# Optimization experiments

Hardware: AMD Instinct MI355X
Metric: run time of the kernel (lower is better)

Reference implementation:

```python
import jax, jax.numpy as jnp
import numpy as np

PATCH = 14          # config.patch_size
MAX_SEQ = 2048      # config.max_vit_seq_len
A2 = 4              # adaptor_patch_size ** 2
GRID = 32           # max_image_size // patch_size -> sqrt(num_positions - 1)
EPS = 1e-5          # layer_norm_eps

IMG_SIZES = [(448, 448), (448, 672), (336, 336), (224, 448), (560, 560), (336, 448)]


def bilinear_resize_chw(img, oh, ow):
    # torch F.interpolate(mode='bilinear', align_corners=False): half-pixel centers, edge clamp
    C, H, W = img.shape
    def coords(o, i):
        c = (jnp.arange(o, dtype=jnp.float32) + 0.5) * (i / o) - 0.5
        c = jnp.clip(c, 0.0, i - 1.0)
        lo = jnp.floor(c).astype(jnp.int32)
        hi = jnp.minimum(lo + 1, i - 1)
        return lo, hi, c - lo
    y0, y1, wy = coords(oh, H)
    x0, x1, wx = coords(ow, W)
    top = img[:, y0][:, :, x0] * (1 - wx) + img[:, y0][:, :, x1] * wx
    bot = img[:, y1][:, :, x0] * (1 - wx) + img[:, y1][:, :, x1] * wx
    wy = wy[None, :, None]
    return top * (1 - wy) + bot * wy


def patch_embed(img, conv_w, conv_b):
    # Conv2d(k=stride=PATCH) == non-overlapping patch extract + matmul
    C, H, W = img.shape
    h, w = H // PATCH, W // PATCH
    x = img[:, :h * PATCH, :w * PATCH].reshape(C, h, PATCH, w, PATCH)
    x = x.transpose(1, 3, 0, 2, 4).reshape(h * w, C * PATCH * PATCH)  # [hw, c*kh*kw]
    out = x @ conv_w.reshape(conv_w.shape[0], -1).T + conv_b          # [hw, E]
    return out, (h, w)


def pos_embed_interp(pos_table, h, w):
    pe = pos_table[1:]  # drop cls position, [GRID*GRID, E]
    if (h, w) == (GRID, GRID):
        return pe
    E = pe.shape[-1]
    pe2d = pe.reshape(GRID, GRID, E).transpose(2, 0, 1)  # [E, GRID, GRID]
    pe2d = bilinear_resize_chw(pe2d, h, w)
    return pe2d.transpose(1, 2, 0).reshape(h * w, E)


def layernorm(x, g, b):
    m = x.mean(-1, keepdims=True)
    v = ((x - m) ** 2).mean(-1, keepdims=True)
    return (x - m) / jnp.sqrt(v + EPS) * g + b


def pack_positions(hw_list):
    # static replay of group_images_by_max_seq_len + a2 rescale in forward
    pos, batch_idx, seq_len = [], 0, 0
    for (h, w) in hw_list:
        L = h * w
        if seq_len + L > MAX_SEQ:
            batch_idx += 1
            seq_len = 0
        s = (seq_len // A2) * A2
        pos.append((batch_idx, s, s + (L // A2) * A2))
        seq_len += L
    return pos, batch_idx + 1


def setup_inputs() -> dict:
    key = jax.random.key(0)
    ks = jax.random.split(key, 9)
    E = 1280
    inp = {}
    for i, (H, W) in enumerate(IMG_SIZES):
        inp[f'img{i}'] = jax.random.normal(ks[i], (3, H, W), dtype=jnp.float32)
    inp['conv_w'] = jax.random.normal(ks[6], (E, 3, PATCH, PATCH), dtype=jnp.float32) * 0.02
    inp['conv_b'] = jnp.zeros((E,), dtype=jnp.float32)
    inp['pos_table'] = jax.random.normal(ks[7], (GRID * GRID + 1, E), dtype=jnp.float32) * 0.02
    inp['ln_w'] = jnp.ones((E,), dtype=jnp.float32)
    inp['ln_b'] = jnp.zeros((E,), dtype=jnp.float32)
    return inp


def reference(img0, img1, img2, img3, img4, img5, conv_w, conv_b, pos_table, ln_w, ln_b):
    images = [img0, img1, img2, img3, img4, img5]
    E = conv_w.shape[0]
    hw = [(im.shape[1] // PATCH, im.shape[2] // PATCH) for im in images]
    positions, B = pack_positions(hw)
    emb = jnp.zeros((B, MAX_SEQ, E), dtype=jnp.float32)
    mask = np.zeros((B, 1, MAX_SEQ, MAX_SEQ), dtype=bool)
    for im, (bi, s, e) in zip(images, positions):
        x, (h, w) = patch_embed(im, conv_w, conv_b)
        x = x + pos_embed_interp(pos_table, h, w)
        x = layernorm(x, ln_w, ln_b)
        emb = emb.at[bi, s:e].set(x)
        mask[bi, 0, s:e, s:e] = True
    return emb, jnp.asarray(mask)
```

## Files before the change

### kernel.cpp

```cpp
#include <hip/hip_runtime.h>
#include <hip/hip_bf16.h>
#include <stdint.h>

#define E_DIM 1280
#define KDIM 588
#define KPAD 608
#define M_TOTAL 6016
#define EMB_FLOATS (5*2048*1280)
#define MASK_FLOATS (5*2048*2048)

#define EXT_BLOCKS  3572
#define CW_BLOCKS   760
#define ZERO_BLOCKS 1320
#define MASK_BLOCKS 5120
#define TOTAL_BLOCKS (EXT_BLOCKS + CW_BLOCKS + ZERO_BLOCKS + MASK_BLOCKS)

typedef __attribute__((ext_vector_type(8))) short bf16x8;
typedef __attribute__((ext_vector_type(4))) float f32x4;

struct us4 { unsigned short x, y, z, w; };

__device__ __forceinline__ unsigned short f2bf(float f) {
    unsigned int u = __float_as_uint(f);
    u += 0x7fff + ((u >> 16) & 1);
    return (unsigned short)(u >> 16);
}

template<int PW, int IMGW, int PLANE>
__device__ __forceinline__ void do_extract4(const float* __restrict__ img,
                                            us4* __restrict__ A4,
                                            int base_u4, int local_u4)
{
    int r_local = local_u4 / 152;
    int k4 = (local_u4 - r_local * 152) * 4;
    us4 v = {0, 0, 0, 0};
    if (k4 < KDIM) {
        int py = r_local / PW;  int px = r_local - py * PW;
        int c   = k4 / 196;
        int rem0 = k4 - c * 196;
        const float* p = img + (size_t)c * PLANE;
        unsigned short o[4];
        #pragma unroll
        for (int j = 0; j < 4; ++j) {
            int rem = rem0 + j;
            int iy = rem / 14, ix = rem - iy * 14;
            o[j] = f2bf(p[(size_t)(py*14 + iy) * IMGW + (px*14 + ix)]);
        }
        v.x = o[0]; v.y = o[1]; v.z = o[2]; v.w = o[3];
    }
    A4[base_u4 + local_u4] = v;
}

__global__ __launch_bounds__(256) void fused_prep(
    const float* __restrict__ i0, const float* __restrict__ i1,
    const float* __restrict__ i2, const float* __restrict__ i3,
    const float* __restrict__ i4, const float* __restrict__ i5,
    const float* __restrict__ conv_w,
    us4* __restrict__ A4, us4* __restrict__ W4,
    float4* __restrict__ out4)
{
    const int bid = blockIdx.x;
    const int t = threadIdx.x;

    if (bid < EXT_BLOCKS) {
        if (bid < 608) {
            do_extract4<32,448,200704>(i0, A4, 0,      bid * 256 + t);
        } else if (bid < 1520) {
            do_extract4<48,672,301056>(i1, A4, 155648, (bid - 608) * 256 + t);
        } else if (bid < 1862) {
            do_extract4<24,336,112896>(i2, A4, 389120, (bid - 1520) * 256 + t);
        } else if (bid < 2166) {
            do_extract4<32,448,100352>(i3, A4, 476672, (bid - 1862) * 256 + t);
        } else if (bid < 3116) {
            do_extract4<40,560,313600>(i4, A4, 554496, (bid - 2166) * 256 + t);
        } else {
            do_extract4<32,448,150528>(i5, A4, 797696, (bid - 3116) * 256 + t);
        }
    } else if (bid < EXT_BLOCKS + CW_BLOCKS) {
        int idx4 = (bid - EXT_BLOCKS) * 256 + t;
        int e  = idx4 / 152;
        int k4 = (idx4 - e * 152) * 4;
        us4 v = {0, 0, 0, 0};
        if (k4 < KDIM) {
            const float* p = conv_w + (size_t)e * KDIM + k4;
            v.x = f2bf(p[0]); v.y = f2bf(p[1]); v.z = f2bf(p[2]); v.w = f2bf(p[3]);
        }
        W4[idx4] = v;
    } else if (bid < EXT_BLOCKS + CW_BLOCKS + ZERO_BLOCKS) {
        int base = (bid - EXT_BLOCKS - CW_BLOCKS) * 1024 + t;
        #pragma unroll
        for (int j = 0; j < 4; ++j) {
            int idx = base + j * 256;
            int zrow = idx / 320;
            int c4   = idx - zrow * 320;
            int b, rowInB;
            if      (zrow < 1024) { b = 0; rowInB = 1024 + zrow; }
            else if (zrow < 1536) { b = 1; rowInB = 1536 + (zrow - 1024); }
            else if (zrow < 2496) { b = 2; rowInB = 1088 + (zrow - 1536); }
            else if (zrow < 2944) { b = 3; rowInB = 1600 + (zrow - 2496); }
            else                  { b = 4; rowInB =  768 + (zrow - 2944); }
            size_t o4 = ((size_t)(b * 2048 + rowInB) * E_DIM) / 4 + c4;
            out4[o4] = make_float4(0.f, 0.f, 0.f, 0.f);
        }
    } else {
        int base = (bid - EXT_BLOCKS - CW_BLOCKS - ZERO_BLOCKS) * 1024 + t;
        #pragma unroll
        for (int j = 0; j < 4; ++j) {
            int m4 = base + j * 256;
            int b  = m4 >> 20;
            int rr = (m4 >> 9) & 2047;
            int c0 = (m4 & 511) * 4;
            int h0 = (b == 0) ? 1024 : (b == 1) ? 1536 : (b == 2) ? 576 : (b == 3) ? 1600 : 768;
            bool on = (rr < h0 && c0 < h0);
            if (b == 2) on = on || (rr >= 576 && rr < 1088 && c0 >= 576 && c0 < 1088);
            float f = on ? 1.f : 0.f;
            out4[(size_t)(EMB_FLOATS / 4) + m4] = make_float4(f, f, f, f);
        }
    }
}

__global__ __launch_bounds__(256) void gemm_bf16(
    const unsigned short* __restrict__ A,
    const unsigned short* __restrict__ Bm,
    float* __restrict__ C)
{
    __shared__ __align__(16) unsigned short As[128*32];
    __shared__ __align__(16) unsigned short Bs[128*32];
    const int t  = threadIdx.x;
    const int m0 = blockIdx.x * 128;
    const int n0 = blockIdx.y * 128;
    const int lane = t & 63;
    const int wv = t >> 6;
    const int wr = wv >> 1, wc = wv & 1;
    const int l16 = lane & 15, q = lane >> 4;

    f32x4 acc[4][4] = {};

    for (int kk = 0; kk < KPAD; kk += 32) {
        #pragma unroll
        for (int i = 0; i < 2; ++i) {
            int off = i * 4096 + t * 16;
            int row = off >> 6;
            int kb  = (off & 63) >> 1;
            const unsigned short* ga = A  + (size_t)(m0 + row) * KPAD + kk + kb;
            __builtin_amdgcn_global_load_lds(
                (const __attribute__((address_space(1))) void*)ga,
                (__attribute__((address_space(3))) void*)((char*)As + off), 16, 0, 0);
            const unsigned short* gb = Bm + (size_t)(n0 + row) * KPAD + kk + kb;
            __builtin_amdgcn_global_load_lds(
                (const __attribute__((address_space(1))) void*)gb,
                (__attribute__((address_space(3))) void*)((char*)Bs + off), 16, 0, 0);
        }
        __syncthreads();

        bf16x8 af[4], bfr[4];
        #pragma unroll
        for (int mi = 0; mi < 4; ++mi)
            af[mi] = *(const bf16x8*)&As[(wr*64 + mi*16 + l16) * 32 + q * 8];
        #pragma unroll
        for (int ni = 0; ni < 4; ++ni)
            bfr[ni] = *(const bf16x8*)&Bs[(wc*64 + ni*16 + l16) * 32 + q * 8];
        #pragma unroll
        for (int mi = 0; mi < 4; ++mi)
            #pragma unroll
            for (int ni = 0; ni < 4; ++ni)
                acc[mi][ni] = __builtin_amdgcn_mfma_f32_16x16x32_bf16(
                    af[mi], bfr[ni], acc[mi][ni], 0, 0, 0);
        __syncthreads();
    }

    #pragma unroll
    for (int mi = 0; mi < 4; ++mi) {
        #pragma unroll
        for (int ni = 0; ni < 4; ++ni) {
            int col = n0 + wc*64 + ni*16 + l16;
            #pragma unroll
            for (int reg = 0; reg < 4; ++reg) {
                int rowr = m0 + wr*64 + mi*16 + q*4 + reg;
                C[(size_t)rowr * E_DIM + col] = acc[mi][ni][reg];
            }
        }
    }
}

__global__ __launch_bounds__(256) void epilogue(
    const float* __restrict__ C, const float* __restrict__ pos_table,
    const float* __restrict__ conv_b,
    const float* __restrict__ ln_w, const float* __restrict__ ln_b,
    float* __restrict__ out)
{
    const int t = threadIdx.x;
    const int wave = t >> 6, lane = t & 63;
    const int r = blockIdx.x * 4 + wave;

    int img     = (r < 1024) ? 0 : (r < 2560) ? 1 : (r < 3136) ? 2 : (r < 3648) ? 3 : (r < 5248) ? 4 : 5;
    int rowOff  = (img == 0) ? 0 : (img == 1) ? 1024 : (img == 2) ? 2560 : (img == 3) ? 3136 : (img == 4) ? 3648 : 5248;
    int h       = (img == 0) ? 32 : (img == 1) ? 32 : (img == 2) ? 24 : (img == 3) ? 16 : (img == 4) ? 40 : 24;
    int w       = (img == 0) ? 32 : (img == 1) ? 48 : (img == 2) ? 24 : (img == 3) ? 32 : (img == 4) ? 40 : 32;
    int outBase = (img == 0) ? 0 : (img == 1) ? 2048 : (img == 2) ? 4096 : (img == 3) ? 4672 : (img == 4) ? 6144 : 8192;

    int ri = r - rowOff;
    int y = ri / w, x = ri - y * w;

    float cy = fminf(fmaxf((y + 0.5f) * (32.0f / h) - 0.5f, 0.0f), 31.0f);
    float cx = fminf(fmaxf((x + 0.5f) * (32.0f / w) - 0.5f, 0.0f), 31.0f);
    int y0 = (int)floorf(cy); int y1 = min(y0 + 1, 31); float wy = cy - (float)y0;
    int x0 = (int)floorf(cx); int x1 = min(x0 + 1, 31); float wx = cx - (float)x0;

    const float4* P00 = (const float4*)(pos_table + (size_t)(1 + y0*32 + x0) * E_DIM);
    const float4* P01 = (const float4*)(pos_table + (size_t)(1 + y0*32 + x1) * E_DIM);
    const float4* P10 = (const float4*)(pos_table + (size_t)(1 + y1*32 + x0) * E_DIM);
    const float4* P11 = (const float4*)(pos_table + (size_t)(1 + y1*32 + x1) * E_DIM);
    const float4* C4  = (const float4*)(C + (size_t)r * E_DIM);
    const float4* B4  = (const float4*)conv_b;

    float w00 = (1.f - wy) * (1.f - wx), w01 = (1.f - wy) * wx;
    float w10 = wy * (1.f - wx),         w11 = wy * wx;

    float4 vals[5];
    float s = 0.f, s2 = 0.f;
    #pragma unroll
    for (int j = 0; j < 5; ++j) {
        int e4 = lane + j * 64;
        float4 a = P00[e4], b2 = P01[e4], c2 = P10[e4], d2 = P11[e4];
        float4 cv = C4[e4], bv = B4[e4];
        float4 v;
        v.x = cv.x + bv.x + w00*a.x + w01*b2.x + w10*c2.x + w11*d2.x;
        v.y = cv.y + bv.y + w00*a.y + w01*b2.y + w10*c2.y + w11*d2.y;
        v.z = cv.z + bv.z + w00*a.z + w01*b2.z + w10*c2.z + w11*d2.z;
        v.w = cv.w + bv.w + w00*a.w + w01*b2.w + w10*c2.w + w11*d2.w;
        vals[j] = v;
        s  += v.x + v.y + v.z + v.w;
        s2 += v.x*v.x + v.y*v.y + v.z*v.z + v.w*v.w;
    }
    #pragma unroll
    for (int m = 32; m > 0; m >>= 1) {
        s  += __shfl_xor(s,  m, 64);
        s2 += __shfl_xor(s2, m, 64);
    }
    float mean = s / 1280.f;
    float var  = s2 / 1280.f - mean * mean;
    float inv  = 1.f / sqrtf(var + 1e-5f);

    float4* O4 = (float4*)(out + (size_t)(outBase + ri) * E_DIM);
    #pragma unroll
    for (int j = 0; j < 5; ++j) {
        int e4 = lane + j * 64;
        float4 g = ((const float4*)ln_w)[e4], be = ((const float4*)ln_b)[e4];
        float4 v = vals[j], o4;
        o4.x = (v.x - mean) * inv * g.x + be.x;
        o4.y = (v.y - mean) * inv * g.y + be.y;
        o4.z = (v.z - mean) * inv * g.z + be.z;
        o4.w = (v.w - mean) * inv * g.w + be.w;
        O4[e4] = o4;
    }
}

extern "C" void kernel_launch(void* const* d_in, const int* in_sizes, int n_in,
                              void* d_out, int out_size, void* d_ws, size_t ws_size,
                              hipStream_t stream) {
    const float* img0 = (const float*)d_in[0];
    const float* img1 = (const float*)d_in[1];
    const float* img2 = (const float*)d_in[2];
    const float* img3 = (const float*)d_in[3];
    const float* img4 = (const float*)d_in[4];
    const float* img5 = (const float*)d_in[5];
    const float* conv_w    = (const float*)d_in[6];
    const float* conv_b    = (const float*)d_in[7];
    const float* pos_table = (const float*)d_in[8];
    const float* ln_w      = (const float*)d_in[9];
    const float* ln_b      = (const float*)d_in[10];
    float* out = (float*)d_out;

    unsigned short* Abf = (unsigned short*)d_ws;
    unsigned short* Wbf = Abf + (size_t)M_TOTAL * KPAD;
    float* Cbuf = (float*)(Wbf + (size_t)E_DIM * KPAD);

    fused_prep<<<TOTAL_BLOCKS, 256, 0, stream>>>(
        img0, img1, img2, img3, img4, img5, conv_w,
        (us4*)Abf, (us4*)Wbf, (float4*)out);

    dim3 g(M_TOTAL / 128, E_DIM / 128);
    gemm_bf16<<<g, 256, 0, stream>>>(Abf, Wbf, Cbuf);

    epilogue<<<1504, 256, 0, stream>>>(Cbuf, pos_table, conv_b, ln_w, ln_b, out);
}
```

Baseline: 206.4 us.

## Fuse GEMM with pos-embed and LayerNorm epilogue, co-schedule mask/zero fill

Replaces the separate LDS-tiled GEMM and epilogue kernels with one kernel. Each block computes a full 32x1280 row strip using direct global-to-register double-buffered fragment loads, then applies bias, bilinear position embedding and LayerNorm in registers with a cross-wave reduction through shared memory. The zero and mask fills move from the prep kernel into this kernel's grid as extra blocks. This drops the fp32 C buffer round trip and one launch. The cost is that the GEMM runs on only 188 blocks and reads unstaged, uncoalesced fragments from global memory.

```diff
diff --git a/kernel.cpp b/kernel.cpp
--- a/kernel.cpp
+++ b/kernel.cpp
@@ -11,9 +11,12 @@
 
 #define EXT_BLOCKS  3572
 #define CW_BLOCKS   760
-#define ZERO_BLOCKS 1320
-#define MASK_BLOCKS 5120
-#define TOTAL_BLOCKS (EXT_BLOCKS + CW_BLOCKS + ZERO_BLOCKS + MASK_BLOCKS)
+#define PREP_BLOCKS (EXT_BLOCKS + CW_BLOCKS)
+
+#define GEMM_BLOCKS 188
+#define ZERO_BLOCKS2 660
+#define MASK_BLOCKS2 2560
+#define FUSED_BLOCKS (GEMM_BLOCKS + ZERO_BLOCKS2 + MASK_BLOCKS2)
 
 typedef __attribute__((ext_vector_type(8))) short bf16x8;
 typedef __attribute__((ext_vector_type(4))) float f32x4;
@@ -51,17 +54,15 @@
     A4[base_u4 + local_u4] = v;
 }
 
-__global__ __launch_bounds__(256) void fused_prep(
+__global__ __launch_bounds__(256) void prep(
     const float* __restrict__ i0, const float* __restrict__ i1,
     const float* __restrict__ i2, const float* __restrict__ i3,
     const float* __restrict__ i4, const float* __restrict__ i5,
     const float* __restrict__ conv_w,
-    us4* __restrict__ A4, us4* __restrict__ W4,
-    float4* __restrict__ out4)
+    us4* __restrict__ A4, us4* __restrict__ W4)
 {
     const int bid = blockIdx.x;
     const int t = threadIdx.x;
-
     if (bid < EXT_BLOCKS) {
         if (bid < 608) {
             do_extract4<32,448,200704>(i0, A4, 0,      bid * 256 + t);
@@ -76,7 +77,7 @@
         } else {
             do_extract4<32,448,150528>(i5, A4, 797696, (bid - 3116) * 256 + t);
         }
-    } else if (bid < EXT_BLOCKS + CW_BLOCKS) {
+    } else {
         int idx4 = (bid - EXT_BLOCKS) * 256 + t;
         int e  = idx4 / 152;
         int k4 = (idx4 - e * 152) * 4;
@@ -86,11 +87,141 @@
             v.x = f2bf(p[0]); v.y = f2bf(p[1]); v.z = f2bf(p[2]); v.w = f2bf(p[3]);
         }
         W4[idx4] = v;
-    } else if (bid < EXT_BLOCKS + CW_BLOCKS + ZERO_BLOCKS) {
-        int base = (bid - EXT_BLOCKS - CW_BLOCKS) * 1024 + t;
+    }
+}
+
+__global__ __launch_bounds__(512) void fused_gemm(
+    const unsigned short* __restrict__ A,
+    const unsigned short* __restrict__ Wb,
+    const float* __restrict__ pos_table, const float* __restrict__ conv_b,
+    const float* __restrict__ ln_w, const float* __restrict__ ln_b,
+    float* __restrict__ out, float4* __restrict__ out4)
+{
+    const int bid = blockIdx.x;
+    const int t = threadIdx.x;
+
+    if (bid < GEMM_BLOCKS) {
+        const int m0   = bid * 32;
+        const int wave = t >> 6;
+        const int lane = t & 63;
+        const int l16  = lane & 15, q = lane >> 4;
+        const int ncol0 = wave * 160;
+
+        f32x4 acc[2][10] = {};
+        const unsigned short* ap = A  + (size_t)(m0 + l16) * KPAD + q * 8;
+        const unsigned short* bp = Wb + (size_t)(ncol0 + l16) * KPAD + q * 8;
+
+        bf16x8 ab[2][2], bb[2][10];
+        #pragma unroll
+        for (int mi = 0; mi < 2; ++mi) ab[0][mi] = *(const bf16x8*)(ap + mi * 16 * KPAD);
+        #pragma unroll
+        for (int ni = 0; ni < 10; ++ni) bb[0][ni] = *(const bf16x8*)(bp + ni * 16 * KPAD);
+
+        #pragma unroll
+        for (int kki = 0; kki < 19; ++kki) {
+            const int cur = kki & 1, nxt = cur ^ 1;
+            if (kki < 18) {
+                const unsigned short* apn = ap + (kki + 1) * 32;
+                const unsigned short* bpn = bp + (kki + 1) * 32;
+                #pragma unroll
+                for (int mi = 0; mi < 2; ++mi) ab[nxt][mi] = *(const bf16x8*)(apn + mi * 16 * KPAD);
+                #pragma unroll
+                for (int ni = 0; ni < 10; ++ni) bb[nxt][ni] = *(const bf16x8*)(bpn + ni * 16 * KPAD);
+            }
+            #pragma unroll
+            for (int mi = 0; mi < 2; ++mi)
+                #pragma unroll
+                for (int ni = 0; ni < 10; ++ni)
+                    acc[mi][ni] = __builtin_amdgcn_mfma_f32_16x16x32_bf16(
+                        ab[cur][mi], bb[cur][ni], acc[mi][ni], 0, 0, 0);
+        }
+
+        int img     = (m0 < 1024) ? 0 : (m0 < 2560) ? 1 : (m0 < 3136) ? 2 : (m0 < 3648) ? 3 : (m0 < 5248) ? 4 : 5;
+        int rowOff  = (img == 0) ? 0 : (img == 1) ? 1024 : (img == 2) ? 2560 : (img == 3) ? 3136 : (img == 4) ? 3648 : 5248;
+        int h       = (img == 0) ? 32 : (img == 1) ? 32 : (img == 2) ? 24 : (img == 3) ? 16 : (img == 4) ? 40 : 24;
+        int w       = (img == 0) ? 32 : (img == 1) ? 48 : (img == 2) ? 24 : (img == 3) ? 32 : (img == 4) ? 40 : 32;
+        int outBase = (img == 0) ? 0 : (img == 1) ? 2048 : (img == 2) ? 4096 : (img == 3) ? 4672 : (img == 4) ? 6144 : 8192;
+        unsigned int magic = (unsigned int)((1u << 22) / (unsigned)w) + 1u;
+        float sh = 32.0f / (float)h, sw = 32.0f / (float)w;
+
+        float cbv[10], gv[10], bev[10];
+        #pragma unroll
+        for (int ni = 0; ni < 10; ++ni) {
+            int col = ncol0 + ni * 16 + l16;
+            cbv[ni] = conv_b[col];
+            gv[ni]  = ln_w[col];
+            bev[ni] = ln_b[col];
+        }
+
+        __shared__ float part_s[8][32], part_s2[8][32], ln_m[32], ln_i[32];
+
+        #pragma unroll
+        for (int mi = 0; mi < 2; ++mi) {
+            #pragma unroll
+            for (int reg = 0; reg < 4; ++reg) {
+                int row_t = mi * 16 + q * 4 + reg;
+                int ri = m0 + row_t - rowOff;
+                unsigned int y = ((unsigned int)ri * magic) >> 22;
+                int x = ri - (int)y * w;
+                float cy = fminf(fmaxf(((float)y + 0.5f) * sh - 0.5f, 0.0f), 31.0f);
+                float cx = fminf(fmaxf(((float)x + 0.5f) * sw - 0.5f, 0.0f), 31.0f);
+                int y0 = (int)cy; int y1 = min(y0 + 1, 31); float wy = cy - (float)y0;
+                int x0 = (int)cx; int x1 = min(x0 + 1, 31); float wx = cx - (float)x0;
+                float w00 = (1.f - wy) * (1.f - wx), w01 = (1.f - wy) * wx;
+                float w10 = wy * (1.f - wx),         w11 = wy * wx;
+                const float* P00 = pos_table + (size_t)(1 + y0*32 + x0) * E_DIM;
+                const float* P01 = pos_table + (size_t)(1 + y0*32 + x1) * E_DIM;
+                const float* P10 = pos_table + (size_t)(1 + y1*32 + x0) * E_DIM;
+                const float* P11 = pos_table + (size_t)(1 + y1*32 + x1) * E_DIM;
+                float s = 0.f, s2 = 0.f;
+                #pragma unroll
+                for (int ni = 0; ni < 10; ++ni) {
+                    int col = ncol0 + ni * 16 + l16;
+                    float p = w00*P00[col] + w01*P01[col] + w10*P10[col] + w11*P11[col];
+                    float v = acc[mi][ni][reg] + cbv[ni] + p;
+                    acc[mi][ni][reg] = v;
+                    s += v; s2 += v * v;
+                }
+                #pragma unroll
+                for (int msk = 1; msk < 16; msk <<= 1) {
+                    s  += __shfl_xor(s,  msk, 64);
+                    s2 += __shfl_xor(s2, msk, 64);
+                }
+                if (l16 == 0) { part_s[wave][row_t] = s; part_s2[wave][row_t] = s2; }
+            }
+        }
+        __syncthreads();
+        if (t < 32) {
+            float S = 0.f, S2 = 0.f;
+            #pragma unroll
+            for (int w2 = 0; w2 < 8; ++w2) { S += part_s[w2][t]; S2 += part_s2[w2][t]; }
+            float mean = S / 1280.f;
+            float var  = S2 / 1280.f - mean * mean;
+            ln_m[t] = mean;
+            ln_i[t] = 1.f / sqrtf(var + 1e-5f);
+        }
+        __syncthreads();
+
+        #pragma unroll
+        for (int mi = 0; mi < 2; ++mi) {
+            #pragma unroll
+            for (int reg = 0; reg < 4; ++reg) {
+                int row_t = mi * 16 + q * 4 + reg;
+                int ri = m0 + row_t - rowOff;
+                float mean = ln_m[row_t], inv = ln_i[row_t];
+                float* orow = out + (size_t)(outBase + ri) * E_DIM;
+                #pragma unroll
+                for (int ni = 0; ni < 10; ++ni) {
+                    int col = ncol0 + ni * 16 + l16;
+                    orow[col] = (acc[mi][ni][reg] - mean) * inv * gv[ni] + bev[ni];
+                }
+            }
+        }
+    } else if (bid < GEMM_BLOCKS + ZERO_BLOCKS2) {
+        int base = (bid - GEMM_BLOCKS) * 2048 + t;
         #pragma unroll
         for (int j = 0; j < 4; ++j) {
-            int idx = base + j * 256;
+            int idx = base + j * 512;
             int zrow = idx / 320;
             int c4   = idx - zrow * 320;
             int b, rowInB;
@@ -103,10 +234,10 @@
             out4[o4] = make_float4(0.f, 0.f, 0.f, 0.f);
         }
     } else {
-        int base = (bid - EXT_BLOCKS - CW_BLOCKS - ZERO_BLOCKS) * 1024 + t;
+        int base = (bid - GEMM_BLOCKS - ZERO_BLOCKS2) * 2048 + t;
         #pragma unroll
         for (int j = 0; j < 4; ++j) {
-            int m4 = base + j * 256;
+            int m4 = base + j * 512;
             int b  = m4 >> 20;
             int rr = (m4 >> 9) & 2047;
             int c0 = (m4 & 511) * 4;
@@ -116,143 +247,6 @@
             float f = on ? 1.f : 0.f;
             out4[(size_t)(EMB_FLOATS / 4) + m4] = make_float4(f, f, f, f);
         }
-    }
-}
-
-__global__ __launch_bounds__(256) void gemm_bf16(
-    const unsigned short* __restrict__ A,
-    const unsigned short* __restrict__ Bm,
-    float* __restrict__ C)
-{
-    __shared__ __align__(16) unsigned short As[128*32];
-    __shared__ __align__(16) unsigned short Bs[128*32];
-    const int t  = threadIdx.x;
-    const int m0 = blockIdx.x * 128;
-    const int n0 = blockIdx.y * 128;
-    const int lane = t & 63;
-    const int wv = t >> 6;
-    const int wr = wv >> 1, wc = wv & 1;
-    const int l16 = lane & 15, q = lane >> 4;
-
-    f32x4 acc[4][4] = {};
-
-    for (int kk = 0; kk < KPAD; kk += 32) {
-        #pragma unroll
-        for (int i = 0; i < 2; ++i) {
-            int off = i * 4096 + t * 16;
-            int row = off >> 6;
-            int kb  = (off & 63) >> 1;
-            const unsigned short* ga = A  + (size_t)(m0 + row) * KPAD + kk + kb;
-            __builtin_amdgcn_global_load_lds(
-                (const __attribute__((address_space(1))) void*)ga,
-                (__attribute__((address_space(3))) void*)((char*)As + off), 16, 0, 0);
-            const unsigned short* gb = Bm + (size_t)(n0 + row) * KPAD + kk + kb;
-            __builtin_amdgcn_global_load_lds(
-                (const __attribute__((address_space(1))) void*)gb,
-                (__attribute__((address_space(3))) void*)((char*)Bs + off), 16, 0, 0);
-        }
-        __syncthreads();
-
-        bf16x8 af[4], bfr[4];
-        #pragma unroll
-        for (int mi = 0; mi < 4; ++mi)
-            af[mi] = *(const bf16x8*)&As[(wr*64 + mi*16 + l16) * 32 + q * 8];
-        #pragma unroll
-        for (int ni = 0; ni < 4; ++ni)
-            bfr[ni] = *(const bf16x8*)&Bs[(wc*64 + ni*16 + l16) * 32 + q * 8];
-        #pragma unroll
-        for (int mi = 0; mi < 4; ++mi)
-            #pragma unroll
-            for (int ni = 0; ni < 4; ++ni)
-                acc[mi][ni] = __builtin_amdgcn_mfma_f32_16x16x32_bf16(
-                    af[mi], bfr[ni], acc[mi][ni], 0, 0, 0);
-        __syncthreads();
-    }
-
-    #pragma unroll
-    for (int mi = 0; mi < 4; ++mi) {
-        #pragma unroll
-        for (int ni = 0; ni < 4; ++ni) {
-            int col = n0 + wc*64 + ni*16 + l16;
-            #pragma unroll
-            for (int reg = 0; reg < 4; ++reg) {
-                int rowr = m0 + wr*64 + mi*16 + q*4 + reg;
-                C[(size_t)rowr * E_DIM + col] = acc[mi][ni][reg];
-            }
-        }
-    }
-}
-
-__global__ __launch_bounds__(256) void epilogue(
-    const float* __restrict__ C, const float* __restrict__ pos_table,
-    const float* __restrict__ conv_b,
-    const float* __restrict__ ln_w, const float* __restrict__ ln_b,
-    float* __restrict__ out)
-{
-    const int t = threadIdx.x;
-    const int wave = t >> 6, lane = t & 63;
-    const int r = blockIdx.x * 4 + wave;
-
-    int img     = (r < 1024) ? 0 : (r < 2560) ? 1 : (r < 3136) ? 2 : (r < 3648) ? 3 : (r < 5248) ? 4 : 5;
-    int rowOff  = (img == 0) ? 0 : (img == 1) ? 1024 : (img == 2) ? 2560 : (img == 3) ? 3136 : (img == 4) ? 3648 : 5248;
-    int h       = (img == 0) ? 32 : (img == 1) ? 32 : (img == 2) ? 24 : (img == 3) ? 16 : (img == 4) ? 40 : 24;
-    int w       = (img == 0) ? 32 : (img == 1) ? 48 : (img == 2) ? 24 : (img == 3) ? 32 : (img == 4) ? 40 : 32;
-    int outBase = (img == 0) ? 0 : (img == 1) ? 2048 : (img == 2) ? 4096 : (img == 3) ? 4672 : (img == 4) ? 6144 : 8192;
-
-    int ri = r - rowOff;
-    int y = ri / w, x = ri - y * w;
-
-    float cy = fminf(fmaxf((y + 0.5f) * (32.0f / h) - 0.5f, 0.0f), 31.0f);
-    float cx = fminf(fmaxf((x + 0.5f) * (32.0f / w) - 0.5f, 0.0f), 31.0f);
-    int y0 = (int)floorf(cy); int y1 = min(y0 + 1, 31); float wy = cy - (float)y0;
-    int x0 = (int)floorf(cx); int x1 = min(x0 + 1, 31); float wx = cx - (float)x0;
-
-    const float4* P00 = (const float4*)(pos_table + (size_t)(1 + y0*32 + x0) * E_DIM);
-    const float4* P01 = (const float4*)(pos_table + (size_t)(1 + y0*32 + x1) * E_DIM);
-    const float4* P10 = (const float4*)(pos_table + (size_t)(1 + y1*32 + x0) * E_DIM);
-    const float4* P11 = (const float4*)(pos_table + (size_t)(1 + y1*32 + x1) * E_DIM);
-    const float4* C4  = (const float4*)(C + (size_t)r * E_DIM);
-    const float4* B4  = (const float4*)conv_b;
-
-    float w00 = (1.f - wy) * (1.f - wx), w01 = (1.f - wy) * wx;
-    float w10 = wy * (1.f - wx),         w11 = wy * wx;
-
-    float4 vals[5];
-    float s = 0.f, s2 = 0.f;
-    #pragma unroll
-    for (int j = 0; j < 5; ++j) {
-        int e4 = lane + j * 64;
-        float4 a = P00[e4], b2 = P01[e4], c2 = P10[e4], d2 = P11[e4];
-        float4 cv = C4[e4], bv = B4[e4];
-        float4 v;
-        v.x = cv.x + bv.x + w00*a.x + w01*b2.x + w10*c2.x + w11*d2.x;
-        v.y = cv.y + bv.y + w00*a.y + w01*b2.y + w10*c2.y + w11*d2.y;
-        v.z = cv.z + bv.z + w00*a.z + w01*b2.z + w10*c2.z + w11*d2.z;
-        v.w = cv.w + bv.w + w00*a.w + w01*b2.w + w10*c2.w + w11*d2.w;
-        vals[j] = v;
-        s  += v.x + v.y + v.z + v.w;
-        s2 += v.x*v.x + v.y*v.y + v.z*v.z + v.w*v.w;
-    }
-    #pragma unroll
-    for (int m = 32; m > 0; m >>= 1) {
-        s  += __shfl_xor(s,  m, 64);
-        s2 += __shfl_xor(s2, m, 64);
-    }
-    float mean = s / 1280.f;
-    float var  = s2 / 1280.f - mean * mean;
-    float inv  = 1.f / sqrtf(var + 1e-5f);
-
-    float4* O4 = (float4*)(out + (size_t)(outBase + ri) * E_DIM);
-    #pragma unroll
-    for (int j = 0; j < 5; ++j) {
-        int e4 = lane + j * 64;
-        float4 g = ((const float4*)ln_w)[e4], be = ((const float4*)ln_b)[e4];
-        float4 v = vals[j], o4;
-        o4.x = (v.x - mean) * inv * g.x + be.x;
-        o4.y = (v.y - mean) * inv * g.y + be.y;
-        o4.z = (v.z - mean) * inv * g.z + be.z;
-        o4.w = (v.w - mean) * inv * g.w + be.w;
-        O4[e4] = o4;
     }
 }
 
@@ -274,14 +268,10 @@
 
     unsigned short* Abf = (unsigned short*)d_ws;
     unsigned short* Wbf = Abf + (size_t)M_TOTAL * KPAD;
-    float* Cbuf = (float*)(Wbf + (size_t)E_DIM * KPAD);
-
-    fused_prep<<<TOTAL_BLOCKS, 256, 0, stream>>>(
-        img0, img1, img2, img3, img4, img5, conv_w,
-        (us4*)Abf, (us4*)Wbf, (float4*)out);
-
-    dim3 g(M_TOTAL / 128, E_DIM / 128);
-    gemm_bf16<<<g, 256, 0, stream>>>(Abf, Wbf, Cbuf);
-
-    epilogue<<<1504, 256, 0, stream>>>(Cbuf, pos_table, conv_b, ln_w, ln_b, out);
-}
+
+    prep<<<PREP_BLOCKS, 256, 0, stream>>>(
+        img0, img1, img2, img3, img4, img5, conv_w, (us4*)Abf, (us4*)Wbf);
+
+    fused_gemm<<<FUSED_BLOCKS, 512, 0, stream>>>(
+        Abf, Wbf, pos_table, conv_b, ln_w, ln_b, out, (float4*)out);
+}
```

New measurement: 203.4 us. About the same (-1.5%).
